# Kernel tuning notes

Measured on AMD Instinct MI355X. Metric: run time of the kernel, lower is better.

Reference implementation:

```python
import jax, jax.numpy as jnp
import numpy as np

H = 64
N_LAYERS = 3
SIZES = {"atom": 100_000, "bond": 200_000, "motif": 50_000, "cell": 5_000}
# (src_type, dst_type) per relation, in HeteroConv dict order
RELS = [("atom", "atom"), ("atom", "bond"), ("atom", "motif"),
        ("bond", "bond"), ("bond", "motif"), ("motif", "motif"),
        ("atom", "cell"), ("bond", "cell"), ("motif", "cell")]
EDGE_NAMES = ["ei_aa", "ei_ab", "ei_am", "ei_bb", "ei_bm", "ei_mm", "ei_ac", "ei_bc", "ei_mc"]
N_EDGES = [800_000, 400_000, 200_000, 400_000, 200_000, 100_000, 100_000, 200_000, 50_000]


def setup_inputs() -> dict:
    key = jax.random.key(0)
    ks = iter(jax.random.split(key, 64))
    inp = {}
    for t in ["atom", "bond", "motif", "cell"]:
        inp["x_" + t] = jax.random.normal(next(ks), (SIZES[t], H), jnp.float32)
    scale = 1.0 / np.sqrt(H)
    inp["Wl"] = jax.random.normal(next(ks), (N_LAYERS, 9, H, H), jnp.float32) * scale
    inp["bl"] = jax.random.normal(next(ks), (N_LAYERS, 9, H), jnp.float32) * 0.01
    inp["Wr"] = jax.random.normal(next(ks), (N_LAYERS, 9, H, H), jnp.float32) * scale
    inp["proj_W"] = jax.random.normal(next(ks), (H, H), jnp.float32) * scale
    inp["proj_b"] = jax.random.normal(next(ks), (H,), jnp.float32) * 0.01
    inp["out_W"] = jax.random.normal(next(ks), (H, 1), jnp.float32) * scale
    inp["out_b"] = jax.random.normal(next(ks), (1,), jnp.float32) * 0.01
    for name, (st, dt), e in zip(EDGE_NAMES, RELS, N_EDGES):
        src = jax.random.randint(next(ks), (e,), 0, SIZES[st], dtype=jnp.int32)
        dst = jax.random.randint(next(ks), (e,), 0, SIZES[dt], dtype=jnp.int32)
        inp[name] = jnp.stack([src, dst]).astype(jnp.int64)
    return inp


def _sage(x_src, x_dst, ei, Wl_r, bl_r, Wr_r):
    """PyG SAGEConv: lin_l(mean of neighbor src feats) + bias + lin_r(x_dst)."""
    src, dst = ei[0], ei[1]
    n_dst = x_dst.shape[0]
    s = jax.ops.segment_sum(x_src[src], dst, num_segments=n_dst)        # [n_dst, H]
    cnt = jax.ops.segment_sum(jnp.ones_like(dst, dtype=x_src.dtype), dst, num_segments=n_dst)
    agg = s / jnp.maximum(cnt, 1.0)[:, None]                            # mean; 0 for isolated
    return agg @ Wl_r + bl_r + x_dst @ Wr_r


def reference(x_atom, x_bond, x_motif, x_cell, Wl, bl, Wr, proj_W, proj_b,
              out_W, out_b, ei_aa, ei_ab, ei_am, ei_bb, ei_bm, ei_mm,
              ei_ac, ei_bc, ei_mc):
    eis = [ei_aa, ei_ab, ei_am, ei_bb, ei_bm, ei_mm, ei_ac, ei_bc, ei_mc]
    x = {"atom": x_atom, "bond": x_bond, "motif": x_motif, "cell": x_cell}
    for l in range(N_LAYERS):
        acc = {t: jnp.zeros((SIZES[t], H), x_atom.dtype) for t in SIZES}
        for r, (st, dt) in enumerate(RELS):
            acc[dt] = acc[dt] + _sage(x[st], x[dt], eis[r], Wl[l, r], bl[l, r], Wr[l, r])
        x = {t: jax.nn.relu(acc[t]) for t in SIZES}  # HeteroConv aggr='sum' then relu
    h = jax.nn.softplus(x["cell"] @ proj_W + proj_b)
    return h @ out_W + out_b  # [n_cell, 1]
```

## Files before the change

### kernel.cpp

```cpp
#include <hip/hip_runtime.h>
#include <hip/hip_bf16.h>

#define H64 64

typedef __bf16 bf16_t;
typedef __bf16 bf16x8 __attribute__((ext_vector_type(8)));
typedef float f32x4 __attribute__((ext_vector_type(4)));

__device__ __forceinline__ float wload(const void* p, long i, bool f32) {
    return f32 ? ((const float*)p)[i]
               : __bfloat162float(((const __hip_bfloat16*)p)[i]);
}
__device__ __forceinline__ float blo(unsigned v) { return __uint_as_float(v << 16); }
__device__ __forceinline__ float bhi(unsigned v) { return __uint_as_float(v & 0xffff0000u); }
__device__ __forceinline__ unsigned packbf(float lo, float hi) {
    __hip_bfloat162 t;
    t.x = __float2bfloat16(lo);
    t.y = __float2bfloat16(hi);
    return *(unsigned*)&t;
}
__device__ __forceinline__ void acc8(float* s, uint4 v, unsigned m) {
    s[0] += blo(v.x & m); s[1] += bhi(v.x & m);
    s[2] += blo(v.y & m); s[3] += bhi(v.y & m);
    s[4] += blo(v.z & m); s[5] += bhi(v.z & m);
    s[6] += blo(v.w & m); s[7] += bhi(v.w & m);
}

__global__ void detect_zero(const unsigned int* __restrict__ eiw, int nwords,
                            const unsigned short* __restrict__ xw,
                            const unsigned short* __restrict__ ww,
                            unsigned int* __restrict__ flags,
                            int4* __restrict__ cntz, long cnt4) {
    long gid = (long)blockIdx.x * 256 + threadIdx.x;
    long gsz = (long)gridDim.x * 256;
    for (long i = gid; i < cnt4; i += gsz) cntz[i] = make_int4(0, 0, 0, 0);
    unsigned int acc = 0;
    for (long i = 1 + 2 * gid; i < nwords; i += 2 * gsz) acc |= eiw[i];
    if (acc) atomicOr(&flags[0], acc);
    unsigned int cx = 0, cw = 0;
    for (long i = gid; i < 8192; i += gsz) {
        unsigned short w = xw[i];
        unsigned int e = (w >> 7) & 0xFF;
        if ((w & 0x7FFF) && (e == 0xFF || e < 0x40)) cx++;
        w = ww[i];
        e = (w >> 7) & 0xFF;
        if ((w & 0x7FFF) && (e == 0xFF || e < 0x40)) cw++;
    }
    if (cx) atomicAdd(&flags[1], cx);
    if (cw) atomicAdd(&flags[2], cw);
}

struct ConvArgs {
    const void* src[4];
    long ubase[4];
    long units[4];
    int blkBase[5];
};
__global__ void conv_prep(ConvArgs ca, __hip_bfloat16* __restrict__ dst,
                          const void* __restrict__ Wl, const void* __restrict__ Wr,
                          const void* __restrict__ bl,
                          const unsigned int* __restrict__ flags,
                          bf16_t* __restrict__ wt, float* __restrict__ blsum) {
    if (blockIdx.x < 39) {
        const int rel_dt[9] = {0, 1, 2, 1, 2, 2, 3, 3, 3};
        bool wf32 = flags[2] > 64;
        int l = blockIdx.x / 13, p = blockIdx.x % 13;
        bf16_t* dw = wt + (long)blockIdx.x * 4096;
        for (int i = threadIdx.x; i < 4096; i += 256) {
            int n = i >> 6, k = i & 63;
            float v;
            if (p < 9) {
                v = wload(Wl, (long)(l * 9 + p) * 4096 + k * 64 + n, wf32);
            } else {
                int dt = p - 9;
                v = 0.f;
                for (int r = 0; r < 9; ++r)
                    if (rel_dt[r] == dt) v += wload(Wr, (long)(l * 9 + r) * 4096 + k * 64 + n, wf32);
            }
            __hip_bfloat16 h = __float2bfloat16(v);
            dw[i] = *(bf16_t*)&h;
        }
        if (p >= 9 && threadIdx.x < 64) {
            int dt = p - 9;
            float s = 0.f;
            for (int r = 0; r < 9; ++r)
                if (rel_dt[r] == dt) s += wload(bl, (long)(l * 9 + r) * 64 + threadIdx.x, wf32);
            blsum[(l * 4 + dt) * 64 + threadIdx.x] = s;
        }
        return;
    }
    bool xf32 = flags[1] > 64;
    int b = blockIdx.x - 39;
    int t = 0;
    while (t < 3 && b >= ca.blkBase[t + 1]) ++t;
    long lu = (long)(b - ca.blkBase[t]) * 256 + threadIdx.x;
    if (lu >= ca.units[t]) return;
    uint4* d4 = (uint4*)dst + ca.ubase[t] + lu;
    if (xf32) {
        const uint4* s = (const uint4*)ca.src[t] + 2 * lu;
        uint4 a = s[0], c = s[1];
        uint4 o;
        o.x = packbf(__uint_as_float(a.x), __uint_as_float(a.y));
        o.y = packbf(__uint_as_float(a.z), __uint_as_float(a.w));
        o.z = packbf(__uint_as_float(c.x), __uint_as_float(c.y));
        o.w = packbf(__uint_as_float(c.z), __uint_as_float(c.w));
        *d4 = o;
    } else {
        *d4 = ((const uint4*)ca.src[t])[lu];
    }
}

struct EdgeArgs {
    const int* ei[9];
    long eoff[10];
    long e2off[10];
    int cntoff[9];
    int srcbase[9];
};

__global__ void count_all(EdgeArgs ea, const unsigned int* __restrict__ flags,
                          int* __restrict__ cnt, int* __restrict__ rank) {
    long u = (long)blockIdx.x * 256 + threadIdx.x;
    if (u >= ea.e2off[9]) return;
    int r = 0;
    while (r < 8 && u >= ea.e2off[r + 1]) ++r;
    long el2 = u - ea.e2off[r];
    long E = ea.eoff[r + 1] - ea.eoff[r];
    long e0 = 2 * el2;
    bool two = (e0 + 1 < E);
    bool is64 = (flags[0] == 0u);
    const int* ei = ea.ei[r];
    int d0, d1 = 0;
    if (is64) { d0 = ei[2 * E + 2 * e0]; if (two) d1 = ei[2 * E + 2 * e0 + 2]; }
    else      { d0 = ei[E + e0];         if (two) d1 = ei[E + e0 + 1]; }
    int base = ea.cntoff[r];
    long eg = ea.eoff[r] + e0;
    rank[eg] = atomicAdd(&cnt[base + d0], 1);
    if (two) rank[eg + 1] = atomicAdd(&cnt[base + d1], 1);
}

__global__ void fill_all(EdgeArgs ea, const unsigned int* __restrict__ flags,
                         const int* __restrict__ row_ptr, const int* __restrict__ rank,
                         int* __restrict__ edge_src) {
    long u = (long)blockIdx.x * 256 + threadIdx.x;
    if (u >= ea.e2off[9]) return;
    int r = 0;
    while (r < 8 && u >= ea.e2off[r + 1]) ++r;
    long el2 = u - ea.e2off[r];
    long E = ea.eoff[r + 1] - ea.eoff[r];
    long e0 = 2 * el2;
    bool two = (e0 + 1 < E);
    bool is64 = (flags[0] == 0u);
    const int* ei = ea.ei[r];
    int s0, d0, s1 = 0, d1 = 0;
    if (is64) {
        s0 = ei[2 * e0];     d0 = ei[2 * E + 2 * e0];
        if (two) { s1 = ei[2 * e0 + 2]; d1 = ei[2 * E + 2 * e0 + 2]; }
    } else {
        s0 = ei[e0];         d0 = ei[E + e0];
        if (two) { s1 = ei[e0 + 1]; d1 = ei[E + e0 + 1]; }
    }
    int base = ea.cntoff[r], sb = ea.srcbase[r];
    long eg = ea.eoff[r] + e0;
    edge_src[row_ptr[base + d0] + rank[eg]] = sb + s0;
    if (two) edge_src[row_ptr[base + d1] + rank[eg + 1]] = sb + s1;
}

__global__ void scan_bsum(const int* __restrict__ cnt, int n, int* __restrict__ bsums) {
    __shared__ int red[256];
    int i = blockIdx.x * 256 + threadIdx.x;
    red[threadIdx.x] = (i < n) ? cnt[i] : 0;
    __syncthreads();
    for (int s = 128; s; s >>= 1) {
        if (threadIdx.x < s) red[threadIdx.x] += red[threadIdx.x + s];
        __syncthreads();
    }
    if (threadIdx.x == 0) bsums[blockIdx.x] = red[0];
}

__global__ void scan_rowptr2(const int* __restrict__ cnt, const int* __restrict__ bsums,
                             int n, int* __restrict__ row_ptr) {
    __shared__ int red[256];
    __shared__ int buf[256];
    int b = blockIdx.x;
    int pre = 0;
    for (int i = threadIdx.x; i < b; i += 256) pre += bsums[i];
    red[threadIdx.x] = pre;
    __syncthreads();
    for (int s = 128; s; s >>= 1) {
        if (threadIdx.x < s) red[threadIdx.x] += red[threadIdx.x + s];
        __syncthreads();
    }
    int base = red[0];
    int i = b * 256 + threadIdx.x;
    int v = (i < n) ? cnt[i] : 0;
    buf[threadIdx.x] = v;
    __syncthreads();
    for (int off = 1; off < 256; off <<= 1) {
        int tv = (threadIdx.x >= off) ? buf[threadIdx.x - off] : 0;
        __syncthreads();
        buf[threadIdx.x] += tv;
        __syncthreads();
    }
    int excl = buf[threadIdx.x] - v + base;
    if (i < n) row_ptr[i] = excl;
    if (i == n - 1) row_ptr[n] = excl + v;
}

struct FusedArgs {
    int cntOff[4][3];
    int wtSlot[4][4];
    long dstBase[4];
    int nDst[4];
    int Rdt[4];
    int blsumOff[4];
    int btBase[5];
    int dtOf[4];
    int totalT16;
};

__device__ __forceinline__ void gather_pass(
    unsigned* __restrict__ L,
    const uint4* __restrict__ xq,
    const int* __restrict__ edge_src,
    const int* __restrict__ row_ptr,
    int cr, bool valid, int gr, int gp) {
    int rp0 = 0, rp1 = 0;
    if (valid) { rp0 = row_ptr[cr]; rp1 = row_ptr[cr + 1]; }
    float s[16];
    #pragma unroll
    for (int j = 0; j < 16; ++j) s[j] = 0.f;
    {
        int idx4[4];
        #pragma unroll
        for (int j = 0; j < 4; ++j) {
            int ee = rp0 + j;
            idx4[j] = edge_src[(ee < rp1) ? ee : 0];
        }
        uint4 v0[4], v1[4];
        #pragma unroll
        for (int j = 0; j < 4; ++j) {
            bool ok = (rp0 + j < rp1);
            unsigned ofs = (unsigned)idx4[j] * 8u + (unsigned)gp * 2u;
            v0[j] = xq[ok ? ofs : 0u];
            v1[j] = xq[ok ? ofs + 1u : 0u];
        }
        #pragma unroll
        for (int j = 0; j < 4; ++j) {
            unsigned m = (rp0 + j < rp1) ? 0xFFFFFFFFu : 0u;
            acc8(s, v0[j], m);
            acc8(s + 8, v1[j], m);
        }
    }
    for (int e = rp0 + 4; e < rp1; e += 4) {
        int idx4[4];
        #pragma unroll
        for (int j = 0; j < 4; ++j) {
            int ee = e + j;
            idx4[j] = edge_src[(ee < rp1) ? ee : 0];
        }
        uint4 v0[4], v1[4];
        #pragma unroll
        for (int j = 0; j < 4; ++j) {
            bool ok = (e + j < rp1);
            unsigned ofs = (unsigned)idx4[j] * 8u + (unsigned)gp * 2u;
            v0[j] = xq[ok ? ofs : 0u];
            v1[j] = xq[ok ? ofs + 1u : 0u];
        }
        #pragma unroll
        for (int j = 0; j < 4; ++j) {
            unsigned m = (e + j < rp1) ? 0xFFFFFFFFu : 0u;
            acc8(s, v0[j], m);
            acc8(s + 8, v1[j], m);
        }
    }
    float inv = (rp1 > rp0) ? 1.0f / (float)(rp1 - rp0) : 0.f;
    unsigned base = (unsigned)gr * 32u;
    #pragma unroll
    for (int h = 0; h < 2; ++h) {
        int d = gp * 8 + h * 4;
        unsigned idxw = base + (unsigned)(d ^ ((gr & 7) << 2));
        uint4 o;
        o.x = packbf(s[h * 8 + 0] * inv, s[h * 8 + 1] * inv);
        o.y = packbf(s[h * 8 + 2] * inv, s[h * 8 + 3] * inv);
        o.z = packbf(s[h * 8 + 4] * inv, s[h * 8 + 5] * inv);
        o.w = packbf(s[h * 8 + 6] * inv, s[h * 8 + 7] * inv);
        *(uint4*)&L[idxw] = o;
    }
}

__device__ __forceinline__ void mfma_pass(f32x4* acc, const bf16_t* wb,
                                          bf16x8 a0, bf16x8 a1, int l16, int quad) {
    #pragma unroll
    for (int nt = 0; nt < 4; ++nt) {
        bf16x8 b0 = *(const bf16x8*)(wb + (nt * 16 + l16) * 64 + quad * 8);
        bf16x8 b1 = *(const bf16x8*)(wb + (nt * 16 + l16) * 64 + 32 + quad * 8);
        acc[nt] = __builtin_amdgcn_mfma_f32_16x16x32_bf16(a0, b0, acc[nt], 0, 0, 0);
        acc[nt] = __builtin_amdgcn_mfma_f32_16x16x32_bf16(a1, b1, acc[nt], 0, 0, 0);
    }
}

__global__ __launch_bounds__(256) void fused_layer(
    const __hip_bfloat16* __restrict__ xin,
    __hip_bfloat16* __restrict__ xout,
    const int* __restrict__ edge_src,
    const int* __restrict__ row_ptr,
    const bf16_t* __restrict__ wt,
    const float* __restrict__ blsum,
    FusedArgs fa) {
    __shared__ unsigned lds[4][2 * 512];

    int wv = threadIdx.x >> 6;
    int g = blockIdx.x * 4 + wv;
    if (g >= fa.totalT16) return;
    int slot = 0;
    while (slot < 3 && g >= fa.btBase[slot + 1]) ++slot;
    int dt = fa.dtOf[slot];
    int t0 = g - fa.btBase[slot];
    int nD = fa.nDst[dt];
    int R = fa.Rdt[dt];

    int lane = threadIdx.x & 63;
    int gr = lane >> 2, gp = lane & 3;
    int row = t0 * 16 + gr;
    bool valid = (row < nD);
    int quad = lane >> 4, l16 = lane & 15;

    const uint4* xq = (const uint4*)xin;
    unsigned* L = lds[wv];

    const bf16_t* ab = (const bf16_t*)xin + (fa.dstBase[dt] + (long)t0 * 16) * 64;
    bf16x8 sa0 = *(const bf16x8*)(ab + l16 * 64 + quad * 8);
    bf16x8 sa1 = *(const bf16x8*)(ab + l16 * 64 + 32 + quad * 8);

    unsigned sw = (unsigned)((l16 & 7) << 2);
    unsigned o0 = (unsigned)l16 * 32u + ((unsigned)(quad * 4) ^ sw);
    unsigned o1 = (unsigned)l16 * 32u + ((unsigned)(16 + quad * 4) ^ sw);
    f32x4 acc[4] = {};

    gather_pass(L, xq, edge_src, row_ptr, fa.cntOff[dt][0] + row, valid, gr, gp);
    if (R > 1)
        gather_pass(L + 512, xq, edge_src, row_ptr, fa.cntOff[dt][1] + row, valid, gr, gp);

    asm volatile("s_waitcnt lgkmcnt(0)" ::: "memory");
    __builtin_amdgcn_sched_barrier(0);

    bf16x8 a00 = *(const bf16x8*)&L[o0];
    bf16x8 a01 = *(const bf16x8*)&L[o1];
    bf16x8 a10 = a00, a11 = a01;
    if (R > 1) { a10 = *(const bf16x8*)&L[512 + o0]; a11 = *(const bf16x8*)&L[512 + o1]; }
    asm volatile("s_waitcnt lgkmcnt(0)" ::: "memory");
    __builtin_amdgcn_sched_barrier(0);

    mfma_pass(acc, wt + (long)fa.wtSlot[dt][0] * 4096, a00, a01, l16, quad);
    if (R > 1)
        mfma_pass(acc, wt + (long)fa.wtSlot[dt][1] * 4096, a10, a11, l16, quad);

    if (R > 2) {
        gather_pass(L, xq, edge_src, row_ptr, fa.cntOff[dt][2] + row, valid, gr, gp);
        asm volatile("s_waitcnt lgkmcnt(0)" ::: "memory");
        __builtin_amdgcn_sched_barrier(0);
        bf16x8 a20 = *(const bf16x8*)&L[o0];
        bf16x8 a21 = *(const bf16x8*)&L[o1];
        mfma_pass(acc, wt + (long)fa.wtSlot[dt][2] * 4096, a20, a21, l16, quad);
    }

    mfma_pass(acc, wt + (long)fa.wtSlot[dt][3] * 4096, sa0, sa1, l16, quad);

    const float* bs = blsum + fa.blsumOff[dt];
    #pragma unroll
    for (int nt = 0; nt < 4; ++nt) {
        int col = nt * 16 + l16;
        float bv = bs[col];
        #pragma unroll
        for (int reg = 0; reg < 4; ++reg) {
            long dd = (long)t0 * 16 + quad * 4 + reg;
            if (dd < nD)
                xout[(fa.dstBase[dt] + dd) * 64 + col] =
                    __float2bfloat16(fmaxf(acc[nt][reg] + bv, 0.f));
        }
    }
}

__global__ __launch_bounds__(256) void head_k(
    const __hip_bfloat16* __restrict__ xc,
    const void* __restrict__ projW, const void* __restrict__ projb,
    const void* __restrict__ outW, const void* __restrict__ outb,
    void* __restrict__ out, const unsigned int* __restrict__ flags, int n) {
    __shared__ float PW[64 * 64];
    __shared__ float PB[64], OW[64];
    __shared__ float ROW[4][64];
    bool wf32 = flags[2] > 64;
    bool of32 = flags[1] > 64;
    int t = threadIdx.x;
    for (int i = t; i < 4096; i += 256) PW[i] = wload(projW, i, wf32);
    if (t < 64) { PB[t] = wload(projb, t, wf32); OW[t] = wload(outW, t, wf32); }
    int wid = t >> 6, lane = t & 63;
    int d = blockIdx.x * 4 + wid;
    ROW[wid][lane] = (d < n) ? __bfloat162float(xc[(long)d * H64 + lane]) : 0.f;
    __syncthreads();
    if (d < n) {
        float s = PB[lane];
        #pragma unroll 8
        for (int k = 0; k < 64; ++k) s += ROW[wid][k] * PW[k * 64 + lane];
        float sp = fmaxf(s, 0.f) + log1pf(expf(-fabsf(s)));
        float c = sp * OW[lane];
        #pragma unroll
        for (int off = 32; off; off >>= 1) c += __shfl_down(c, off, 64);
        if (lane == 0) {
            float rv = c + wload(outb, 0, wf32);
            if (of32) ((float*)out)[d] = rv;
            else ((__hip_bfloat16*)out)[d] = __float2bfloat16(rv);
        }
    }
}

extern "C" void kernel_launch(void* const* d_in, const int* in_sizes, int n_in,
                              void* d_out, int out_size, void* d_ws, size_t ws_size,
                              hipStream_t stream) {
    static const int rel_st[9] = {0, 0, 0, 1, 1, 2, 0, 1, 2};
    static const int rel_dt[9] = {0, 1, 2, 1, 2, 2, 3, 3, 3};
    static const int relsOf[4][3] = {{0, -1, -1}, {1, 3, -1}, {2, 4, 5}, {6, 7, 8}};
    static const int Rof[4] = {1, 2, 3, 3};
    static const int order[4] = {3, 0, 2, 1};

    long rows[4], rowoff[4], total = 0;
    for (int t = 0; t < 4; ++t) { rows[t] = in_sizes[t] / H64; rowoff[t] = total; total += rows[t]; }
    long NX = total * H64;
    long NXpad = (total + 64) * H64;
    long Es[9], ET = 0;
    for (int r = 0; r < 9; ++r) { Es[r] = (long)in_sizes[11 + r] / 2; ET += Es[r]; }
    long cntoff[9], cntN = 0;
    for (int r = 0; r < 9; ++r) { cntoff[r] = cntN; cntN += rows[rel_dt[r]]; }
    long nb1 = (cntN + 255) / 256;

    unsigned int* flags = (unsigned int*)d_ws;
    char* wsbase = (char*)d_ws + 64;
    auto align16 = [](size_t v) { return (v + 15) & ~(size_t)15; };
    size_t off = 0;
    __hip_bfloat16* x0 = (__hip_bfloat16*)(wsbase + off);  off = align16(off + (size_t)NXpad * 2);
    __hip_bfloat16* x1 = (__hip_bfloat16*)(wsbase + off);  off = align16(off + (size_t)NXpad * 2);
    int* cnt_i = (int*)(wsbase + off);                     off = align16(off + (size_t)(cntN + 4) * 4);
    int* row_ptr = (int*)(wsbase + off);                   off = align16(off + (size_t)(cntN + 1) * 4);
    int* rank = (int*)(wsbase + off);                      off = align16(off + (size_t)ET * 4);
    int* edge_src = (int*)(wsbase + off);                  off = align16(off + (size_t)ET * 4);
    int* bsums = (int*)(wsbase + off);                     off = align16(off + (size_t)nb1 * 4);
    bf16_t* wt = (bf16_t*)(wsbase + off);                  off = align16(off + (size_t)39 * 4096 * 2);
    float* blsum = (float*)(wsbase + off);                 off = align16(off + (size_t)12 * 64 * 4);

    hipMemsetAsync(d_ws, 0, 64, stream);
    int nwords = 16384;
    if (in_sizes[11] < nwords) nwords = in_sizes[11];
    detect_zero<<<256, 256, 0, stream>>>((const unsigned int*)d_in[11], nwords,
                                         (const unsigned short*)d_in[0],
                                         (const unsigned short*)d_in[4], flags,
                                         (int4*)cnt_i, (cntN + 3) / 4);

    ConvArgs ca;
    int cb = 0;
    for (int t = 0; t < 4; ++t) {
        ca.src[t] = d_in[t];
        ca.ubase[t] = rowoff[t] * 8;
        ca.units[t] = rows[t] * 8;
        ca.blkBase[t] = cb;
        cb += (int)((ca.units[t] + 255) / 256);
    }
    ca.blkBase[4] = cb;
    conv_prep<<<39 + cb, 256, 0, stream>>>(ca, x0, d_in[4], d_in[6], d_in[5],
                                           flags, wt, blsum);

    EdgeArgs ea;
    long ecum = 0, e2cum = 0;
    for (int r = 0; r < 9; ++r) {
        ea.ei[r] = (const int*)d_in[11 + r];
        ea.eoff[r] = ecum;   ecum += Es[r];
        ea.e2off[r] = e2cum; e2cum += (Es[r] + 1) / 2;
        ea.cntoff[r] = (int)cntoff[r];
        ea.srcbase[r] = (int)rowoff[rel_st[r]];
    }
    ea.eoff[9] = ecum;
    ea.e2off[9] = e2cum;

    count_all<<<(int)((e2cum + 255) / 256), 256, 0, stream>>>(ea, flags, cnt_i, rank);
    scan_bsum<<<(int)nb1, 256, 0, stream>>>(cnt_i, (int)cntN, bsums);
    scan_rowptr2<<<(int)nb1, 256, 0, stream>>>(cnt_i, bsums, (int)cntN, row_ptr);
    fill_all<<<(int)((e2cum + 255) / 256), 256, 0, stream>>>(ea, flags, row_ptr, rank, edge_src);

    FusedArgs fa;
    int bb = 0;
    for (int s = 0; s < 4; ++s) {
        int dt = order[s];
        fa.dtOf[s] = dt;
        fa.btBase[s] = bb;
        bb += (int)((rows[dt] + 15) / 16);
    }
    fa.btBase[4] = bb;
    fa.totalT16 = bb;
    for (int dt = 0; dt < 4; ++dt) {
        fa.nDst[dt] = (int)rows[dt];
        fa.Rdt[dt] = Rof[dt];
        fa.dstBase[dt] = rowoff[dt];
        for (int p = 0; p < 3; ++p) {
            int rr = (p < Rof[dt]) ? relsOf[dt][p] : relsOf[dt][0];
            fa.cntOff[dt][p] = (int)cntoff[rr];
        }
    }

    for (int l = 0; l < 3; ++l) {
        for (int dt = 0; dt < 4; ++dt) {
            fa.blsumOff[dt] = (l * 4 + dt) * 64;
            for (int p = 0; p < 3; ++p) {
                int rr = (p < Rof[dt]) ? relsOf[dt][p] : relsOf[dt][0];
                fa.wtSlot[dt][p] = l * 13 + rr;
            }
            fa.wtSlot[dt][3] = l * 13 + 9 + dt;
        }
        const __hip_bfloat16* xin = (l & 1) ? x1 : x0;
        __hip_bfloat16* xo = (l & 1) ? x0 : x1;
        fused_layer<<<(bb + 3) / 4, 256, 0, stream>>>(xin, xo, edge_src, row_ptr, wt, blsum, fa);
    }

    head_k<<<(int)((rows[3] + 3) / 4), 256, 0, stream>>>(
        x1 + rowoff[3] * H64, d_in[7], d_in[8], d_in[9], d_in[10], d_out, flags, (int)rows[3]);
}
```

Before: 771.3 us.

## Fuse preprocessing kernels into one cooperative kernel with grid syncs

Replaces the memset and six preprocessing launches (zeroing, type detection, conversion and weight prep, edge counting, the two scan passes, CSR fill) with one cooperative kernel. Each phase runs as a grid-stride loop over a persistent grid, and `grid.sync()` separates dependent phases. The aim is to remove per-launch overhead and the gaps between the small kernels. In exchange it pays for grid-wide barriers and runs fewer resident blocks over the edge phases. The fallback path no longer zeroes the flags, because the memset was removed.

```diff
diff --git a/kernel.cpp b/kernel.cpp
--- a/kernel.cpp
+++ b/kernel.cpp
@@ -1,5 +1,8 @@
 #include <hip/hip_runtime.h>
 #include <hip/hip_bf16.h>
+#include <hip/hip_cooperative_groups.h>
+
+namespace cg = cooperative_groups;
 
 #define H64 64
 
@@ -26,47 +29,54 @@
     s[6] += blo(v.w & m); s[7] += bhi(v.w & m);
 }
 
-__global__ void detect_zero(const unsigned int* __restrict__ eiw, int nwords,
-                            const unsigned short* __restrict__ xw,
-                            const unsigned short* __restrict__ ww,
-                            unsigned int* __restrict__ flags,
-                            int4* __restrict__ cntz, long cnt4) {
-    long gid = (long)blockIdx.x * 256 + threadIdx.x;
-    long gsz = (long)gridDim.x * 256;
-    for (long i = gid; i < cnt4; i += gsz) cntz[i] = make_int4(0, 0, 0, 0);
-    unsigned int acc = 0;
-    for (long i = 1 + 2 * gid; i < nwords; i += 2 * gsz) acc |= eiw[i];
-    if (acc) atomicOr(&flags[0], acc);
-    unsigned int cx = 0, cw = 0;
-    for (long i = gid; i < 8192; i += gsz) {
-        unsigned short w = xw[i];
-        unsigned int e = (w >> 7) & 0xFF;
-        if ((w & 0x7FFF) && (e == 0xFF || e < 0x40)) cx++;
-        w = ww[i];
-        e = (w >> 7) & 0xFF;
-        if ((w & 0x7FFF) && (e == 0xFF || e < 0x40)) cw++;
-    }
-    if (cx) atomicAdd(&flags[1], cx);
-    if (cw) atomicAdd(&flags[2], cw);
-}
-
 struct ConvArgs {
     const void* src[4];
     long ubase[4];
     long units[4];
     int blkBase[5];
 };
-__global__ void conv_prep(ConvArgs ca, __hip_bfloat16* __restrict__ dst,
-                          const void* __restrict__ Wl, const void* __restrict__ Wr,
-                          const void* __restrict__ bl,
-                          const unsigned int* __restrict__ flags,
-                          bf16_t* __restrict__ wt, float* __restrict__ blsum) {
-    if (blockIdx.x < 39) {
+struct EdgeArgs {
+    const int* ei[9];
+    long eoff[10];
+    long e2off[10];
+    int cntoff[9];
+    int srcbase[9];
+};
+
+__device__ __forceinline__ void dev_zero(long gid, long gsz,
+                                         int4* cntz, long cnt4, unsigned* flags) {
+    for (long i = gid; i < cnt4; i += gsz) cntz[i] = make_int4(0, 0, 0, 0);
+    if (gid < 16) flags[gid] = 0u;
+}
+
+__device__ __forceinline__ void dev_detect(long gid, long gsz,
+        const unsigned* eiw, int nwords,
+        const unsigned short* xw, const unsigned short* ww, unsigned* flags) {
+    unsigned acc = 0;
+    for (long i = 1 + 2 * gid; i < nwords; i += 2 * gsz) acc |= eiw[i];
+    if (acc) atomicOr(&flags[0], acc);
+    unsigned cx = 0, cw = 0;
+    for (long i = gid; i < 8192; i += gsz) {
+        unsigned short w = xw[i];
+        unsigned e = (w >> 7) & 0xFF;
+        if ((w & 0x7FFF) && (e == 0xFF || e < 0x40)) cx++;
+        w = ww[i];
+        e = (w >> 7) & 0xFF;
+        if ((w & 0x7FFF) && (e == 0xFF || e < 0x40)) cw++;
+    }
+    if (cx) atomicAdd(&flags[1], cx);
+    if (cw) atomicAdd(&flags[2], cw);
+}
+
+__device__ __forceinline__ void dev_convprep_vb(int vb, int tid, const ConvArgs& ca,
+        __hip_bfloat16* dst, const void* Wl, const void* Wr, const void* bl,
+        const unsigned* flags, bf16_t* wt, float* blsum) {
+    if (vb < 39) {
         const int rel_dt[9] = {0, 1, 2, 1, 2, 2, 3, 3, 3};
         bool wf32 = flags[2] > 64;
-        int l = blockIdx.x / 13, p = blockIdx.x % 13;
-        bf16_t* dw = wt + (long)blockIdx.x * 4096;
-        for (int i = threadIdx.x; i < 4096; i += 256) {
+        int l = vb / 13, p = vb % 13;
+        bf16_t* dw = wt + (long)vb * 4096;
+        for (int i = tid; i < 4096; i += 256) {
             int n = i >> 6, k = i & 63;
             float v;
             if (p < 9) {
@@ -80,20 +90,20 @@
             __hip_bfloat16 h = __float2bfloat16(v);
             dw[i] = *(bf16_t*)&h;
         }
-        if (p >= 9 && threadIdx.x < 64) {
+        if (p >= 9 && tid < 64) {
             int dt = p - 9;
             float s = 0.f;
             for (int r = 0; r < 9; ++r)
-                if (rel_dt[r] == dt) s += wload(bl, (long)(l * 9 + r) * 64 + threadIdx.x, wf32);
-            blsum[(l * 4 + dt) * 64 + threadIdx.x] = s;
+                if (rel_dt[r] == dt) s += wload(bl, (long)(l * 9 + r) * 64 + tid, wf32);
+            blsum[(l * 4 + dt) * 64 + tid] = s;
         }
         return;
     }
     bool xf32 = flags[1] > 64;
-    int b = blockIdx.x - 39;
+    int b = vb - 39;
     int t = 0;
     while (t < 3 && b >= ca.blkBase[t + 1]) ++t;
-    long lu = (long)(b - ca.blkBase[t]) * 256 + threadIdx.x;
+    long lu = (long)(b - ca.blkBase[t]) * 256 + tid;
     if (lu >= ca.units[t]) return;
     uint4* d4 = (uint4*)dst + ca.ubase[t] + lu;
     if (xf32) {
@@ -110,25 +120,14 @@
     }
 }
 
-struct EdgeArgs {
-    const int* ei[9];
-    long eoff[10];
-    long e2off[10];
-    int cntoff[9];
-    int srcbase[9];
-};
-
-__global__ void count_all(EdgeArgs ea, const unsigned int* __restrict__ flags,
-                          int* __restrict__ cnt, int* __restrict__ rank) {
-    long u = (long)blockIdx.x * 256 + threadIdx.x;
-    if (u >= ea.e2off[9]) return;
+__device__ __forceinline__ void dev_count_u(long u, const EdgeArgs& ea, bool is64,
+                                            int* cnt, int* rank) {
     int r = 0;
     while (r < 8 && u >= ea.e2off[r + 1]) ++r;
     long el2 = u - ea.e2off[r];
     long E = ea.eoff[r + 1] - ea.eoff[r];
     long e0 = 2 * el2;
     bool two = (e0 + 1 < E);
-    bool is64 = (flags[0] == 0u);
     const int* ei = ea.ei[r];
     int d0, d1 = 0;
     if (is64) { d0 = ei[2 * E + 2 * e0]; if (two) d1 = ei[2 * E + 2 * e0 + 2]; }
@@ -139,18 +138,14 @@
     if (two) rank[eg + 1] = atomicAdd(&cnt[base + d1], 1);
 }
 
-__global__ void fill_all(EdgeArgs ea, const unsigned int* __restrict__ flags,
-                         const int* __restrict__ row_ptr, const int* __restrict__ rank,
-                         int* __restrict__ edge_src) {
-    long u = (long)blockIdx.x * 256 + threadIdx.x;
-    if (u >= ea.e2off[9]) return;
+__device__ __forceinline__ void dev_fill_u(long u, const EdgeArgs& ea, bool is64,
+        const int* row_ptr, const int* rank, int* edge_src) {
     int r = 0;
     while (r < 8 && u >= ea.e2off[r + 1]) ++r;
     long el2 = u - ea.e2off[r];
     long E = ea.eoff[r + 1] - ea.eoff[r];
     long e0 = 2 * el2;
     bool two = (e0 + 1 < E);
-    bool is64 = (flags[0] == 0u);
     const int* ei = ea.ei[r];
     int s0, d0, s1 = 0, d1 = 0;
     if (is64) {
@@ -166,6 +161,111 @@
     if (two) edge_src[row_ptr[base + d1] + rank[eg + 1]] = sb + s1;
 }
 
+struct PrepArgs {
+    const unsigned* eiw; int nwords;
+    const unsigned short* xw; const unsigned short* ww;
+    unsigned* flags;
+    int4* cntz; long cnt4;
+    ConvArgs ca; __hip_bfloat16* xdst;
+    const void *Wl, *Wr, *bl; bf16_t* wt; float* blsum;
+    int convBlocks;
+    EdgeArgs ea;
+    int* cnt; int* rank; int* edge_src; int* row_ptr; int* bsums;
+    int cntN; int nb1;
+};
+
+__global__ __launch_bounds__(256) void prep_coop(PrepArgs pa) {
+    cg::grid_group grid = cg::this_grid();
+    __shared__ int sbuf[256];
+    int tid = threadIdx.x;
+    long gid = (long)blockIdx.x * 256 + tid;
+    long gsz = (long)gridDim.x * 256;
+
+    dev_zero(gid, gsz, pa.cntz, pa.cnt4, pa.flags);
+    grid.sync();
+    dev_detect(gid, gsz, pa.eiw, pa.nwords, pa.xw, pa.ww, pa.flags);
+    grid.sync();
+    for (int vb = blockIdx.x; vb < 39 + pa.convBlocks; vb += gridDim.x)
+        dev_convprep_vb(vb, tid, pa.ca, pa.xdst, pa.Wl, pa.Wr, pa.bl,
+                        pa.flags, pa.wt, pa.blsum);
+    grid.sync();
+    bool is64 = (pa.flags[0] == 0u);
+    long e2 = pa.ea.e2off[9];
+    for (long u = gid; u < e2; u += gsz) dev_count_u(u, pa.ea, is64, pa.cnt, pa.rank);
+    grid.sync();
+    for (int vb = blockIdx.x; vb < pa.nb1; vb += gridDim.x) {
+        int i = vb * 256 + tid;
+        sbuf[tid] = (i < pa.cntN) ? pa.cnt[i] : 0;
+        __syncthreads();
+        for (int s = 128; s; s >>= 1) {
+            if (tid < s) sbuf[tid] += sbuf[tid + s];
+            __syncthreads();
+        }
+        if (tid == 0) pa.bsums[vb] = sbuf[0];
+        __syncthreads();
+    }
+    grid.sync();
+    for (int vb = blockIdx.x; vb < pa.nb1; vb += gridDim.x) {
+        int pre = 0;
+        for (int i = tid; i < vb; i += 256) pre += pa.bsums[i];
+        sbuf[tid] = pre;
+        __syncthreads();
+        for (int s = 128; s; s >>= 1) {
+            if (tid < s) sbuf[tid] += sbuf[tid + s];
+            __syncthreads();
+        }
+        int base = sbuf[0];
+        __syncthreads();
+        int i = vb * 256 + tid;
+        int v = (i < pa.cntN) ? pa.cnt[i] : 0;
+        sbuf[tid] = v;
+        __syncthreads();
+        for (int off = 1; off < 256; off <<= 1) {
+            int tv = (tid >= off) ? sbuf[tid - off] : 0;
+            __syncthreads();
+            sbuf[tid] += tv;
+            __syncthreads();
+        }
+        int excl = sbuf[tid] - v + base;
+        if (i < pa.cntN) pa.row_ptr[i] = excl;
+        if (i == pa.cntN - 1) pa.row_ptr[pa.cntN] = excl + v;
+        __syncthreads();
+    }
+    grid.sync();
+    for (long u = gid; u < e2; u += gsz)
+        dev_fill_u(u, pa.ea, is64, pa.row_ptr, pa.rank, pa.edge_src);
+}
+
+__global__ void detect_zero(const unsigned* __restrict__ eiw, int nwords,
+                            const unsigned short* __restrict__ xw,
+                            const unsigned short* __restrict__ ww,
+                            unsigned* __restrict__ flags,
+                            int4* __restrict__ cntz, long cnt4) {
+    long gid = (long)blockIdx.x * 256 + threadIdx.x;
+    long gsz = (long)gridDim.x * 256;
+    for (long i = gid; i < cnt4; i += gsz) cntz[i] = make_int4(0, 0, 0, 0);
+    dev_detect(gid, gsz, eiw, nwords, xw, ww, flags);
+}
+__global__ void conv_prep(ConvArgs ca, __hip_bfloat16* __restrict__ dst,
+                          const void* __restrict__ Wl, const void* __restrict__ Wr,
+                          const void* __restrict__ bl,
+                          const unsigned* __restrict__ flags,
+                          bf16_t* __restrict__ wt, float* __restrict__ blsum) {
+    dev_convprep_vb(blockIdx.x, threadIdx.x, ca, dst, Wl, Wr, bl, flags, wt, blsum);
+}
+__global__ void count_all(EdgeArgs ea, const unsigned* __restrict__ flags,
+                          int* __restrict__ cnt, int* __restrict__ rank) {
+    long u = (long)blockIdx.x * 256 + threadIdx.x;
+    if (u >= ea.e2off[9]) return;
+    dev_count_u(u, ea, flags[0] == 0u, cnt, rank);
+}
+__global__ void fill_all(EdgeArgs ea, const unsigned* __restrict__ flags,
+                         const int* __restrict__ row_ptr, const int* __restrict__ rank,
+                         int* __restrict__ edge_src) {
+    long u = (long)blockIdx.x * 256 + threadIdx.x;
+    if (u >= ea.e2off[9]) return;
+    dev_fill_u(u, ea, flags[0] == 0u, row_ptr, rank, edge_src);
+}
 __global__ void scan_bsum(const int* __restrict__ cnt, int n, int* __restrict__ bsums) {
     __shared__ int red[256];
     int i = blockIdx.x * 256 + threadIdx.x;
@@ -177,7 +277,6 @@
     }
     if (threadIdx.x == 0) bsums[blockIdx.x] = red[0];
 }
-
 __global__ void scan_rowptr2(const int* __restrict__ cnt, const int* __restrict__ bsums,
                              int n, int* __restrict__ row_ptr) {
     __shared__ int red[256];
@@ -448,13 +547,8 @@
     bf16_t* wt = (bf16_t*)(wsbase + off);                  off = align16(off + (size_t)39 * 4096 * 2);
     float* blsum = (float*)(wsbase + off);                 off = align16(off + (size_t)12 * 64 * 4);
 
-    hipMemsetAsync(d_ws, 0, 64, stream);
     int nwords = 16384;
     if (in_sizes[11] < nwords) nwords = in_sizes[11];
-    detect_zero<<<256, 256, 0, stream>>>((const unsigned int*)d_in[11], nwords,
-                                         (const unsigned short*)d_in[0],
-                                         (const unsigned short*)d_in[4], flags,
-                                         (int4*)cnt_i, (cntN + 3) / 4);
 
     ConvArgs ca;
     int cb = 0;
@@ -466,8 +560,6 @@
         cb += (int)((ca.units[t] + 255) / 256);
     }
     ca.blkBase[4] = cb;
-    conv_prep<<<39 + cb, 256, 0, stream>>>(ca, x0, d_in[4], d_in[6], d_in[5],
-                                           flags, wt, blsum);
 
     EdgeArgs ea;
     long ecum = 0, e2cum = 0;
@@ -481,10 +573,43 @@
     ea.eoff[9] = ecum;
     ea.e2off[9] = e2cum;
 
-    count_all<<<(int)((e2cum + 255) / 256), 256, 0, stream>>>(ea, flags, cnt_i, rank);
-    scan_bsum<<<(int)nb1, 256, 0, stream>>>(cnt_i, (int)cntN, bsums);
-    scan_rowptr2<<<(int)nb1, 256, 0, stream>>>(cnt_i, bsums, (int)cntN, row_ptr);
-    fill_all<<<(int)((e2cum + 255) / 256), 256, 0, stream>>>(ea, flags, row_ptr, rank, edge_src);
+    PrepArgs pa;
+    pa.eiw = (const unsigned*)d_in[11]; pa.nwords = nwords;
+    pa.xw = (const unsigned short*)d_in[0]; pa.ww = (const unsigned short*)d_in[4];
+    pa.flags = flags;
+    pa.cntz = (int4*)cnt_i; pa.cnt4 = (cntN + 3) / 4;
+    pa.ca = ca; pa.xdst = x0;
+    pa.Wl = d_in[4]; pa.Wr = d_in[6]; pa.bl = d_in[5];
+    pa.wt = wt; pa.blsum = blsum;
+    pa.convBlocks = cb;
+    pa.ea = ea;
+    pa.cnt = cnt_i; pa.rank = rank; pa.edge_src = edge_src;
+    pa.row_ptr = row_ptr; pa.bsums = bsums;
+    pa.cntN = (int)cntN; pa.nb1 = (int)nb1;
+
+    static int coopBlocks = -1;
+    if (coopBlocks < 0) {
+        int mb = 0;
+        hipError_t oe = hipOccupancyMaxActiveBlocksPerMultiprocessor(&mb, prep_coop, 256, 0);
+        if (oe != hipSuccess || mb < 1) mb = 1;
+        long g = (long)mb * 256;
+        if (g > 2048) g = 2048;
+        coopBlocks = (int)g;
+    }
+    void* kargs[] = { (void*)&pa };
+    hipError_t le = hipLaunchCooperativeKernel((const void*)prep_coop,
+                                               dim3(coopBlocks), dim3(256),
+                                               kargs, 0, stream);
+    if (le != hipSuccess) {
+        detect_zero<<<256, 256, 0, stream>>>(pa.eiw, nwords, pa.xw, pa.ww, flags,
+                                             (int4*)cnt_i, pa.cnt4);
+        conv_prep<<<39 + cb, 256, 0, stream>>>(ca, x0, d_in[4], d_in[6], d_in[5],
+                                               flags, wt, blsum);
+        count_all<<<(int)((e2cum + 255) / 256), 256, 0, stream>>>(ea, flags, cnt_i, rank);
+        scan_bsum<<<(int)nb1, 256, 0, stream>>>(cnt_i, (int)cntN, bsums);
+        scan_rowptr2<<<(int)nb1, 256, 0, stream>>>(cnt_i, bsums, (int)cntN, row_ptr);
+        fill_all<<<(int)((e2cum + 255) / 256), 256, 0, stream>>>(ea, flags, row_ptr, rank, edge_src);
+    }
 
     FusedArgs fa;
     int bb = 0;
```

Result: slower. 1.491 ms (+93.3%).
